# Performance work log

Measured on AMD Instinct MI355X. Metric: run time of the kernel, lower is better.

The kernel has to match this reference:

```python
import jax, jax.numpy as jnp
import numpy as np

T = 2048      # number of utterances in the dialogue (sequential loop dim)
L = 50        # tokens per utterance
V = 30000     # vocab size
D = 300       # word embedding dim
NF = 64       # CNN filters per width
H = 100       # hidden size (hard-coded in CMN)
NC = 7        # emotion classes
WIND = 40     # args.wind1 sliding memory window
HOPS = 3      # args.hops
NEG = -1e10   # masked_fill value in dotprod_attention


def setup_inputs() -> dict:
    key = jax.random.key(0)
    ks = jax.random.split(key, 24)
    s = 0.05

    def n(k, shape):
        return jax.random.normal(k, shape, jnp.float32) * s

    return {
        "sents": jax.random.randint(ks[0], (T, L), 0, V, dtype=jnp.int32),
        "lengths": jax.random.randint(ks[1], (T,), 1, L, dtype=jnp.int32),
        "emb": n(ks[2], (V, D)),
        "Wc3": n(ks[3], (NF, 1, 3, D)), "bc3": n(ks[4], (NF,)),
        "Wc4": n(ks[5], (NF, 1, 4, D)), "bc4": n(ks[6], (NF,)),
        "Wc5": n(ks[7], (NF, 1, 5, D)), "bc5": n(ks[8], (NF,)),
        "Wt": n(ks[9], (3 * NF, H)), "bt": n(ks[10], (H,)),
        "Wih_c": n(ks[11], (3 * H, H)), "Whh_c": n(ks[12], (3 * H, H)),
        "bih_c": n(ks[13], (3 * H,)), "bhh_c": n(ks[14], (3 * H,)),
        "Wih_m": n(ks[15], (3 * H, H)), "Whh_m": n(ks[16], (3 * H, H)),
        "bih_m": n(ks[17], (3 * H,)), "bhh_m": n(ks[18], (3 * H,)),
        "Wcls": n(ks[19], (H, NC)), "bcls": n(ks[20], (NC,)),
    }


def _gru_cell(x, h, Wih, Whh, bih, bhh):
    # torch GRU cell, gate order (r, z, n)
    gi = x @ Wih.T + bih
    gh = h @ Whh.T + bhh
    ir, iz, inn = jnp.split(gi, 3, axis=-1)
    hr, hz, hn = jnp.split(gh, 3, axis=-1)
    r = jax.nn.sigmoid(ir + hr)
    z = jax.nn.sigmoid(iz + hz)
    nw = jnp.tanh(inn + r * hn)
    return (1.0 - z) * nw + z * h


def reference(sents, lengths, emb, Wc3, bc3, Wc4, bc4, Wc5, bc5, Wt, bt,
              Wih_c, Whh_c, bih_c, bhh_c, Wih_m, Whh_m, bih_m, bhh_m,
              Wcls, bcls):
    # ---- CNN utterance encoder (dropout layers are identity in eval) ----
    w = emb[sents]                       # (T, L, D)
    x = w[:, None]                       # (T, 1, L, D)  NCHW
    feats = []
    for Wc, bc in ((Wc3, bc3), (Wc4, bc4), (Wc5, bc5)):
        y = jax.lax.conv_general_dilated(
            x, Wc, window_strides=(1, 1), padding='VALID',
            dimension_numbers=('NCHW', 'OIHW', 'NCHW'))  # (T, NF, L-fs+1, 1)
        feats.append(jnp.max(jax.nn.relu(y + bc[None, :, None, None]), axis=(2, 3)))
    s_utt = jnp.tanh(jnp.concatenate(feats, axis=1) @ Wt + bt)  # (T, H)

    # ---- context GRU over utterances 0..T-2 (hidden after torch step i is hiddens[i-1]) ----
    def cont_step(h, u):
        h2 = _gru_cell(u, h, Wih_c, Whh_c, bih_c, bhh_c)
        return h2, h2
    _, hiddens = jax.lax.scan(cont_step, jnp.zeros((H,), jnp.float32), s_utt[:-1])  # (T-1, H)

    # ---- sliding memory windows: step i (1..T-1) sees hiddens[i-WIND .. i-1], newest last ----
    idx = jnp.arange(1, T)[:, None] - WIND + jnp.arange(WIND)[None, :]  # (T-1, WIND)
    valid = idx >= 0
    mem_all = jnp.where(valid[..., None], hiddens[jnp.clip(idx, 0)], 0.0)  # (T-1, WIND, H)

    def attend(query, mem, v):
        # query: (H,), mem: (WIND, H), v: (WIND,) bool
        for _ in range(HOPS):
            scores = jnp.where(v, mem @ query, NEG)
            a = jax.nn.softmax(scores)
            query = jnp.tanh(query + a @ mem)
            if HOPS > 1:
                # mem_gru over the valid suffix of the window (zero init hidden,
                # padded slots skipped so recurrence starts at first valid slot)
                def mstep(hm, xv):
                    xx, vv = xv
                    hn = _gru_cell(xx, hm, Wih_m, Whh_m, bih_m, bhh_m)
                    hm = jnp.where(vv, hn, hm)
                    return hm, hm
                _, mem = jax.lax.scan(mstep, jnp.zeros((H,), jnp.float32), (mem, v))
        return query

    queries = jax.vmap(attend)(s_utt[1:], mem_all, valid)       # (T-1, H)
    s_cont = jnp.concatenate([s_utt[:1], queries], axis=0)      # (T, H)
    logits = s_cont @ Wcls + bcls                                # (T, NC)
    return jax.nn.log_softmax(logits, axis=1)
```

## Files before the change

kernel.cpp:

```cpp
#include <hip/hip_runtime.h>

#define TT 2048
#define LL 50
#define DD 300
#define HH 100
#define NCC 7

typedef unsigned short u16;
typedef unsigned int u32;
typedef _Float16 f16x2 __attribute__((ext_vector_type(2)));
typedef _Float16 f16x8 __attribute__((ext_vector_type(8)));
typedef float f32x4 __attribute__((ext_vector_type(4)));

__device__ __forceinline__ float frcp(float x){ return __builtin_amdgcn_rcpf(x); }
__device__ __forceinline__ float sigm(float x){ return frcp(1.f + __expf(-x)); }
__device__ __forceinline__ float ftanh(float x){ return 1.f - 2.f * frcp(1.f + __expf(2.f * x)); }

#if defined(__has_builtin)
#if __has_builtin(__builtin_amdgcn_fdot2)
#define HAS_FDOT2 1
#endif
#endif
__device__ __forceinline__ float fdot2(f16x2 a, f16x2 b, float c){
#ifdef HAS_FDOT2
  return __builtin_amdgcn_fdot2(a, b, c, false);
#else
  return c + (float)a.x * (float)b.x + (float)a.y * (float)b.y;
#endif
}
__device__ __forceinline__ f16x2 pk(float x, float y){ f16x2 r; r.x = (_Float16)x; r.y = (_Float16)y; return r; }

__global__ __launch_bounds__(256) void k_prep(const float* __restrict__ Wc3,
    const float* __restrict__ Wc4, const float* __restrict__ Wc5, _Float16* __restrict__ wtp)
{
  const int t = blockIdx.x;
  int kki, ntile, kt;
  if (t < 120){ kki = 0; ntile = t / 30;        kt = t % 30; }
  else if (t < 280){ kki = 1; int r = t - 120; ntile = r / 40; kt = r % 40; }
  else { kki = 2; int r = t - 280;             ntile = r / 50; kt = r % 50; }
  const float* W = (kki == 0) ? Wc3 : ((kki == 1) ? Wc4 : Wc5);
  const int kk = 3 + kki;
  #pragma unroll
  for (int u = 0; u < 2; ++u){
    int e = threadIdx.x * 2 + u;
    int lane = e >> 3, i = e & 7;
    int k = kt * 32 + (lane >> 4) * 8 + i;
    int f = ntile * 16 + (lane & 15);
    int j = k / 320, d = k - j * 320;
    float v = (d < DD) ? W[((size_t)f * kk + j) * DD + d] : 0.f;
    wtp[(size_t)t * 512 + e] = (_Float16)v;
  }
}

#define WST 328
__global__ __launch_bounds__(256) void k_cnn(const int* __restrict__ sents,
    const float* __restrict__ emb, const _Float16* __restrict__ wtp,
    const float* __restrict__ bc3, const float* __restrict__ bc4, const float* __restrict__ bc5,
    const float* __restrict__ Wt,  const float* __restrict__ bt,
    float* __restrict__ su)
{
  __shared__ __attribute__((aligned(16))) _Float16 w16[52 * WST];
  __shared__ float feats[192];
  __shared__ int ids[LL];
  const int tid = threadIdx.x;
  const int s = blockIdx.x;

  if (tid < LL) ids[tid] = sents[s * LL + tid];
  for (int e = tid; e < 52 * WST / 2; e += 256) ((u32*)w16)[e] = 0u;
  __syncthreads();
  for (int e = tid; e < LL * 75; e += 256){
    int l = e / 75, d4 = (e - l * 75) * 4;
    float4 v = *(const float4*)&emb[(size_t)ids[l] * DD + d4];
    _Float16* p = &w16[l * WST + d4];
    p[0] = (_Float16)v.x; p[1] = (_Float16)v.y; p[2] = (_Float16)v.z; p[3] = (_Float16)v.w;
  }
  __syncthreads();

  const int lane = tid & 63, wid = tid >> 6;
  const int rl = lane & 15, gp = lane >> 4;
  const int kkstart[3] = {0, 120, 280};
  float fmaxv[3];
  #pragma unroll
  for (int kki = 0; kki < 3; ++kki){
    const int kk = 3 + kki, nkt = kk * 10, Pk = LL - kk + 1;
    f32x4 acc0 = {0.f,0.f,0.f,0.f}, acc1 = acc0, acc2 = acc0;
    const f16x8* bp = (const f16x8*)(wtp + (size_t)(kkstart[kki] + wid * nkt) * 512) + lane;
    int j = 0, d = gp * 8;
    for (int kt = 0; kt < nkt; ++kt){
      f16x8 b  = bp[(size_t)kt * 64];
      f16x8 a0 = *(const f16x8*)&w16[(rl      + j) * WST + d];
      f16x8 a1 = *(const f16x8*)&w16[(16 + rl + j) * WST + d];
      f16x8 a2 = *(const f16x8*)&w16[(32 + rl + j) * WST + d];
      acc0 = __builtin_amdgcn_mfma_f32_16x16x32_f16(a0, b, acc0, 0, 0, 0);
      acc1 = __builtin_amdgcn_mfma_f32_16x16x32_f16(a1, b, acc1, 0, 0, 0);
      acc2 = __builtin_amdgcn_mfma_f32_16x16x32_f16(a2, b, acc2, 0, 0, 0);
      d += 32; if (d >= 320){ d -= 320; ++j; }
    }
    float m = -1e30f;
    #pragma unroll
    for (int r = 0; r < 4; ++r){
      int p0 = gp * 4 + r;
      if (p0 < Pk)      m = fmaxf(m, acc0[r]);
      if (16 + p0 < Pk) m = fmaxf(m, acc1[r]);
      if (32 + p0 < Pk) m = fmaxf(m, acc2[r]);
    }
    m = fmaxf(m, __shfl_xor(m, 16));
    m = fmaxf(m, __shfl_xor(m, 32));
    fmaxv[kki] = m;
  }
  if (lane < 16){
    feats[  0 + wid * 16 + lane] = fmaxv[0];
    feats[ 64 + wid * 16 + lane] = fmaxv[1];
    feats[128 + wid * 16 + lane] = fmaxv[2];
  }
  __syncthreads();
  if (tid < 192){
    float bias = (tid < 64) ? bc3[tid] : ((tid < 128) ? bc4[tid - 64] : bc5[tid - 128]);
    feats[tid] = fmaxf(0.f, feats[tid] + bias);
  }
  __syncthreads();
  if (tid < HH){
    float acc = bt[tid];
    for (int c = 0; c < 192; ++c)
      acc += feats[c] * Wt[c * HH + tid];
    su[(size_t)s * HH + tid] = ftanh(acc);
  }
}

__global__ __launch_bounds__(320) void k_gi(const float* __restrict__ src,
    const float* __restrict__ W, const float* __restrict__ b, float* __restrict__ dst)
{
  __shared__ float x[HH];
  const int t = blockIdx.x, tid = threadIdx.x;
  if (tid < HH) x[tid] = src[(size_t)t * HH + tid];
  __syncthreads();
  if (tid < 300){
    float acc = b[tid];
    const float* wr = W + (size_t)tid * HH;
    #pragma unroll
    for (int i = 0; i < 25; ++i){
      float4 wv = *(const float4*)(wr + 4 * i);
      float4 xv = *(const float4*)&x[4 * i];
      acc += xv.x * wv.x + xv.y * wv.y + xv.z * wv.z + xv.w * wv.w;
    }
    dst[(size_t)t * 300 + tid] = acc;
  }
}

#define CH 16
__global__ __launch_bounds__(320, 1) void k_scan(const float* __restrict__ gi,
    const float* __restrict__ Whh, const float* __restrict__ bhh,
    float* __restrict__ hid, int steps)
{
  __shared__ __attribute__((aligned(16))) _Float16 h16[104];
  __shared__ float gh_l[300];
  __shared__ float gi_buf[CH * 300];
  __shared__ float hid_buf[CH * HH];
  const int tid = threadIdx.x;
  f16x2 wv[52];
  float bh = 0.f, hreg = 0.f;
  if (tid < 300){
    const float* r0 = Whh + (size_t)tid * 100;
    #pragma unroll
    for (int i = 0; i < 25; ++i){
      float4 a = *(const float4*)(r0 + 4 * i);
      wv[2*i] = pk(a.x, a.y); wv[2*i+1] = pk(a.z, a.w);
    }
    bh = bhh[tid];
  }
  wv[50] = pk(0,0); wv[51] = pk(0,0);
  if (tid < 104) h16[tid] = (_Float16)0.f;
  {
    int c0 = (steps < CH ? steps : CH) * 75;
    for (int e = tid; e < c0; e += 320)
      ((float4*)gi_buf)[e] = ((const float4*)gi)[e];
  }
  __syncthreads();

  int t0 = 0;
  while (t0 < steps){
    int cnt = steps - t0; if (cnt > CH) cnt = CH;
    for (int s = 0; s < cnt; ++s){
      if (tid < 300){
        float a0 = 0, a1 = 0;
        const float4* hq = (const float4*)h16;
        #pragma unroll
        for (int g = 0; g < 13; ++g){
          float4 hv = hq[g];
          a0 = fdot2(wv[4*g  ], __builtin_bit_cast(f16x2, hv.x), a0);
          a1 = fdot2(wv[4*g+1], __builtin_bit_cast(f16x2, hv.y), a1);
          a0 = fdot2(wv[4*g+2], __builtin_bit_cast(f16x2, hv.z), a0);
          a1 = fdot2(wv[4*g+3], __builtin_bit_cast(f16x2, hv.w), a1);
        }
        gh_l[tid] = a0 + a1 + bh;
      }
      __syncthreads();
      if (tid < HH){
        const float* gp = gi_buf + s * 300;
        float r = sigm(gp[tid]       + gh_l[tid]);
        float z = sigm(gp[tid + 100] + gh_l[tid + 100]);
        float n = ftanh(gp[tid + 200] + r * gh_l[tid + 200]);
        float o = (1.f - z) * n + z * hreg;
        hreg = o;
        h16[tid] = (_Float16)o;
        hid_buf[s * HH + tid] = o;
      }
      __syncthreads();
    }
    for (int e = tid; e < cnt * 25; e += 320)
      ((float4*)(hid + (size_t)t0 * HH))[e] = ((const float4*)hid_buf)[e];
    int nt0 = t0 + cnt;
    int ncnt = steps - nt0; if (ncnt > CH) ncnt = CH; if (ncnt < 0) ncnt = 0;
    for (int e = tid; e < ncnt * 75; e += 320)
      ((float4*)gi_buf)[e] = ((const float4*)(gi + (size_t)nt0 * 300))[e];
    __syncthreads();
    t0 = nt0;
  }
}

__global__ __launch_bounds__(320) void k_att(
    const float* __restrict__ su, const float* __restrict__ hid, const float* __restrict__ gm,
    const float* __restrict__ Wih, const float* __restrict__ Whh,
    const float* __restrict__ bih, const float* __restrict__ bhh,
    float* __restrict__ scont)
{
  __shared__ float mem_l[40 * 104];
  __shared__ __attribute__((aligned(16))) _Float16 mem16[40 * 104];
  __shared__ float hbuf[HH];
  __shared__ __attribute__((aligned(16))) _Float16 hb16[104];
  __shared__ float gh_l[300];
  __shared__ float q_l[104];
  __shared__ float sc_l[40];
  __shared__ float bi_l[300];
  __shared__ _Float16 g_l[40 * 300];
  const int tid = threadIdx.x;
  const int q = blockIdx.x;
  int wmin = 39 - q; if (wmin < 0) wmin = 0;
  f16x2 wreg[52];
  float bh = 0.f;

  if (tid < 300){ bi_l[tid] = bih[tid]; bh = bhh[tid]; }
  if (tid < 104) q_l[tid] = (tid < 100) ? su[(size_t)(q + 1) * HH + tid] : 0.f;
  for (int e = tid; e < 40 * 104; e += 320){
    int w = e / 104, i = e - w * 104;
    float v = 0.f;
    if (i < 100 && w >= wmin) v = hid[(size_t)(q - 39 + w) * HH + i];
    mem_l[e] = v;
    mem16[e] = (_Float16)v;
  }
  for (int e = tid; e < 40 * 300; e += 320){
    int w = e / 300, j = e - w * 300;
    float v = (w >= wmin) ? gm[(size_t)(q - 39 + w) * 300 + j] : 0.f;
    g_l[e] = (_Float16)v;
  }
  if (tid < 300){
    const float* r0 = Whh + (size_t)tid * 100;
    #pragma unroll
    for (int i = 0; i < 25; ++i){
      float4 a = *(const float4*)(r0 + 4 * i);
      wreg[2*i] = pk(a.x, a.y); wreg[2*i+1] = pk(a.z, a.w);
    }
  }
  wreg[50] = pk(0,0); wreg[51] = pk(0,0);
  __syncthreads();

  for (int hop = 0; hop < 3; ++hop){
    if (tid < 40){
      float a0 = 0, a1 = 0, a2 = 0, a3 = 0;
      const float* mr = &mem_l[tid * 104];
      #pragma unroll
      for (int i = 0; i < 25; ++i){
        float4 m4 = *(const float4*)&mr[4 * i];
        float4 q4 = *(const float4*)&q_l[4 * i];
        a0 += m4.x * q4.x; a1 += m4.y * q4.y; a2 += m4.z * q4.z; a3 += m4.w * q4.w;
      }
      sc_l[tid] = (tid >= wmin) ? ((a0 + a1) + (a2 + a3)) : -1e10f;
    }
    __syncthreads();
    if (tid < 64){
      float v = (tid < 40) ? sc_l[tid] : -3e38f;
      float m = v;
      #pragma unroll
      for (int off = 32; off; off >>= 1) m = fmaxf(m, __shfl_xor(m, off));
      float e = (tid < 40) ? __expf(v - m) : 0.f;
      float ssum = e;
      #pragma unroll
      for (int off = 32; off; off >>= 1) ssum += __shfl_xor(ssum, off);
      if (tid < 40) sc_l[tid] = e * frcp(ssum);
    }
    __syncthreads();
    if (tid < 50){
      float c0 = 0.f, c1 = 0.f;
      for (int w = wmin; w < 40; ++w){
        float a = sc_l[w];
        float2 mv = *(const float2*)&mem_l[w * 104 + 2 * tid];
        c0 += a * mv.x; c1 += a * mv.y;
      }
      float q0 = ftanh(q_l[2 * tid]     + c0);
      float q1 = ftanh(q_l[2 * tid + 1] + c1);
      *(float2*)&q_l[2 * tid] = make_float2(q0, q1);
      if (hop == 2)
        *(float2*)&scont[(size_t)(q + 1) * HH + 2 * tid] = make_float2(q0, q1);
    }
    if (hop == 2) break;

    if (hop == 1){
      if (tid < 300){
        const float* r0 = Wih + (size_t)tid * 100;
        #pragma unroll
        for (int i = 0; i < 25; ++i){
          float4 a = *(const float4*)(r0 + 4 * i);
          wreg[2*i] = pk(a.x, a.y); wreg[2*i+1] = pk(a.z, a.w);
        }
        for (int w = 0; w < 40; ++w){
          float a0 = 0, a1 = 0;
          const float4* mq = (const float4*)&mem16[w * 104];
          #pragma unroll
          for (int g = 0; g < 13; ++g){
            float4 hv = mq[g];
            a0 = fdot2(wreg[4*g  ], __builtin_bit_cast(f16x2, hv.x), a0);
            a1 = fdot2(wreg[4*g+1], __builtin_bit_cast(f16x2, hv.y), a1);
            a0 = fdot2(wreg[4*g+2], __builtin_bit_cast(f16x2, hv.z), a0);
            a1 = fdot2(wreg[4*g+3], __builtin_bit_cast(f16x2, hv.w), a1);
          }
          g_l[w * 300 + tid] = (_Float16)(a0 + a1 + bi_l[tid]);
        }
        const float* rh = Whh + (size_t)tid * 100;
        #pragma unroll
        for (int i = 0; i < 25; ++i){
          float4 a = *(const float4*)(rh + 4 * i);
          wreg[2*i] = pk(a.x, a.y); wreg[2*i+1] = pk(a.z, a.w);
        }
      }
    }

    if (tid < HH) hbuf[tid] = 0.f;
    if (tid < 104) hb16[tid] = (_Float16)0.f;
    __syncthreads();
    for (int w = 0; w < 40; ++w){
      if (tid < 300){
        float a0 = 0, a1 = 0;
        const float4* hq = (const float4*)hb16;
        #pragma unroll
        for (int g = 0; g < 13; ++g){
          float4 hv = hq[g];
          a0 = fdot2(wreg[4*g  ], __builtin_bit_cast(f16x2, hv.x), a0);
          a1 = fdot2(wreg[4*g+1], __builtin_bit_cast(f16x2, hv.y), a1);
          a0 = fdot2(wreg[4*g+2], __builtin_bit_cast(f16x2, hv.z), a0);
          a1 = fdot2(wreg[4*g+3], __builtin_bit_cast(f16x2, hv.w), a1);
        }
        gh_l[tid] = a0 + a1 + bh;
      }
      __syncthreads();
      if (tid < HH){
        float o = hbuf[tid];
        if (w >= wmin){
          const _Float16* gp = &g_l[w * 300];
          float gir = (float)gp[tid], giz = (float)gp[tid + 100], gin = (float)gp[tid + 200];
          float r = sigm(gir + gh_l[tid]);
          float z = sigm(giz + gh_l[tid + 100]);
          float n = ftanh(gin + r * gh_l[tid + 200]);
          o = (1.f - z) * n + z * o;
        }
        hbuf[tid] = o;
        hb16[tid] = (_Float16)o;
        mem_l[w * 104 + tid] = o;
        mem16[w * 104 + tid] = (_Float16)o;
      }
      __syncthreads();
    }
  }
}

__global__ __launch_bounds__(256) void k_cls(const float* __restrict__ su, const float* __restrict__ scont,
    const float* __restrict__ Wcls, const float* __restrict__ bcls, float* __restrict__ out)
{
  __shared__ float wl[HH * NCC];
  __shared__ float bl[NCC];
  const int tid = threadIdx.x;
  for (int e = tid; e < HH * NCC; e += 256) wl[e] = Wcls[e];
  if (tid < NCC) bl[tid] = bcls[tid];
  __syncthreads();
  int r = blockIdx.x * 256 + tid;
  if (r < TT){
    const float* v = (r == 0) ? su : (scont + (size_t)r * HH);
    float l[NCC];
    #pragma unroll
    for (int c = 0; c < NCC; ++c) l[c] = bl[c];
    for (int h = 0; h < HH; ++h){
      float x = v[h];
      #pragma unroll
      for (int c = 0; c < NCC; ++c) l[c] += x * wl[h * NCC + c];
    }
    float m = l[0];
    #pragma unroll
    for (int c = 1; c < NCC; ++c) m = fmaxf(m, l[c]);
    float ssum = 0.f;
    #pragma unroll
    for (int c = 0; c < NCC; ++c) ssum += __expf(l[c] - m);
    float lse = m + __logf(ssum);
    #pragma unroll
    for (int c = 0; c < NCC; ++c) out[(size_t)r * NCC + c] = l[c] - lse;
  }
}

extern "C" void kernel_launch(void* const* d_in, const int* in_sizes, int n_in,
                              void* d_out, int out_size, void* d_ws, size_t ws_size,
                              hipStream_t stream)
{
  const int* sents  = (const int*)d_in[0];
  const float* emb    = (const float*)d_in[2];
  const float* Wc3    = (const float*)d_in[3];  const float* bc3 = (const float*)d_in[4];
  const float* Wc4    = (const float*)d_in[5];  const float* bc4 = (const float*)d_in[6];
  const float* Wc5    = (const float*)d_in[7];  const float* bc5 = (const float*)d_in[8];
  const float* Wt     = (const float*)d_in[9];  const float* bt  = (const float*)d_in[10];
  const float* Wih_c  = (const float*)d_in[11]; const float* Whh_c = (const float*)d_in[12];
  const float* bih_c  = (const float*)d_in[13]; const float* bhh_c = (const float*)d_in[14];
  const float* Wih_m  = (const float*)d_in[15]; const float* Whh_m = (const float*)d_in[16];
  const float* bih_m  = (const float*)d_in[17]; const float* bhh_m = (const float*)d_in[18];
  const float* Wcls   = (const float*)d_in[19]; const float* bcls  = (const float*)d_in[20];

  float* ws    = (float*)d_ws;
  float* su    = ws;
  float* gic   = su  + 204800;
  float* hid   = gic + 614100;
  float* gm    = gic;
  float* scont = hid + 204700;
  _Float16* wtp = (_Float16*)(scont + 204800);

  k_prep<<<480,     256, 0, stream>>>(Wc3, Wc4, Wc5, wtp);
  k_cnn <<<TT,      256, 0, stream>>>(sents, emb, wtp, bc3, bc4, bc5, Wt, bt, su);
  k_gi  <<<TT - 1,  320, 0, stream>>>(su, Wih_c, bih_c, gic);
  k_scan<<<1,       320, 0, stream>>>(gic, Whh_c, bhh_c, hid, TT - 1);
  k_gi  <<<TT - 1,  320, 0, stream>>>(hid, Wih_m, bih_m, gm);
  k_att <<<TT - 1,  320, 0, stream>>>(su, hid, gm, Wih_m, Whh_m, bih_m, bhh_m, scont);
  k_cls <<<(TT + 255) / 256, 256, 0, stream>>>(su, scont, Wcls, bcls, (float*)d_out);
}
```

Measured before the change: 1.996 ms.

## Remap GRU scan lanes so gates exchange via DPP, one barrier per step

The sequential GRU scan kernel now places the r/z/n gate rows for one hidden unit in adjacent lanes of a quad, using 448 threads. Gate values are exchanged with DPP quad broadcasts instead of going through shared memory. The hidden-state buffer is double-buffered, so each timestep needs one __syncthreads instead of two. This targets barrier and LDS round-trip latency on the serial critical path, at the cost of more threads and redundant gate math in idle lanes.

```diff
diff --git a/kernel.cpp b/kernel.cpp
--- a/kernel.cpp
+++ b/kernel.cpp
@@ -29,6 +29,12 @@
 #endif
 }
 __device__ __forceinline__ f16x2 pk(float x, float y){ f16x2 r; r.x = (_Float16)x; r.y = (_Float16)y; return r; }
+
+template<int CTRL>
+__device__ __forceinline__ float qb(float x){
+  return __builtin_bit_cast(float,
+    __builtin_amdgcn_mov_dpp(__builtin_bit_cast(int, x), CTRL, 0xF, 0xF, true));
+}
 
 __global__ __launch_bounds__(256) void k_prep(const float* __restrict__ Wc3,
     const float* __restrict__ Wc4, const float* __restrict__ Wc5, _Float16* __restrict__ wtp)
@@ -148,31 +154,36 @@
 }
 
 #define CH 16
-__global__ __launch_bounds__(320, 1) void k_scan(const float* __restrict__ gi,
+__global__ __launch_bounds__(448, 1) void k_scan(const float* __restrict__ gi,
     const float* __restrict__ Whh, const float* __restrict__ bhh,
     float* __restrict__ hid, int steps)
 {
-  __shared__ __attribute__((aligned(16))) _Float16 h16[104];
-  __shared__ float gh_l[300];
+  __shared__ __attribute__((aligned(16))) _Float16 hA[104];
+  __shared__ __attribute__((aligned(16))) _Float16 hB[104];
   __shared__ float gi_buf[CH * 300];
   __shared__ float hid_buf[CH * HH];
   const int tid = threadIdx.x;
+  const int w = tid >> 6, l = tid & 63;
+  const int u = w * 16 + (l >> 2), g = l & 3;
+  const bool act = (u < HH) && (g < 3);
+  const int row = act ? (u + 100 * g) : 0;
+  const int gidx = act ? (u + 100 * g) : 0;
   f16x2 wv[52];
   float bh = 0.f, hreg = 0.f;
-  if (tid < 300){
-    const float* r0 = Whh + (size_t)tid * 100;
+  {
+    const float* r0 = Whh + (size_t)row * 100;
     #pragma unroll
     for (int i = 0; i < 25; ++i){
       float4 a = *(const float4*)(r0 + 4 * i);
       wv[2*i] = pk(a.x, a.y); wv[2*i+1] = pk(a.z, a.w);
     }
-    bh = bhh[tid];
+    bh = bhh[row];
   }
   wv[50] = pk(0,0); wv[51] = pk(0,0);
-  if (tid < 104) h16[tid] = (_Float16)0.f;
+  if (tid < 104){ hA[tid] = (_Float16)0.f; hB[tid] = (_Float16)0.f; }
   {
     int c0 = (steps < CH ? steps : CH) * 75;
-    for (int e = tid; e < c0; e += 320)
+    for (int e = tid; e < c0; e += 448)
       ((float4*)gi_buf)[e] = ((const float4*)gi)[e];
   }
   __syncthreads();
@@ -181,37 +192,38 @@
   while (t0 < steps){
     int cnt = steps - t0; if (cnt > CH) cnt = CH;
     for (int s = 0; s < cnt; ++s){
-      if (tid < 300){
-        float a0 = 0, a1 = 0;
-        const float4* hq = (const float4*)h16;
-        #pragma unroll
-        for (int g = 0; g < 13; ++g){
-          float4 hv = hq[g];
-          a0 = fdot2(wv[4*g  ], __builtin_bit_cast(f16x2, hv.x), a0);
-          a1 = fdot2(wv[4*g+1], __builtin_bit_cast(f16x2, hv.y), a1);
-          a0 = fdot2(wv[4*g+2], __builtin_bit_cast(f16x2, hv.z), a0);
-          a1 = fdot2(wv[4*g+3], __builtin_bit_cast(f16x2, hv.w), a1);
-        }
-        gh_l[tid] = a0 + a1 + bh;
+      const _Float16* hs = ((t0 + s) & 1) ? hB : hA;
+      _Float16*       hd = ((t0 + s) & 1) ? hA : hB;
+      float giv = gi_buf[s * 300 + gidx];
+      float a0 = 0, a1 = 0;
+      const float4* hq = (const float4*)hs;
+      #pragma unroll
+      for (int gg = 0; gg < 13; ++gg){
+        float4 hv = hq[gg];
+        a0 = fdot2(wv[4*gg  ], __builtin_bit_cast(f16x2, hv.x), a0);
+        a1 = fdot2(wv[4*gg+1], __builtin_bit_cast(f16x2, hv.y), a1);
+        a0 = fdot2(wv[4*gg+2], __builtin_bit_cast(f16x2, hv.z), a0);
+        a1 = fdot2(wv[4*gg+3], __builtin_bit_cast(f16x2, hv.w), a1);
+      }
+      float gh = a0 + a1 + bh;
+      float ghr = qb<0x00>(gh),  ghz = qb<0x55>(gh),  ghn = qb<0xAA>(gh);
+      float gir = qb<0x00>(giv), giz = qb<0x55>(giv), gin = qb<0xAA>(giv);
+      float r = sigm(gir + ghr);
+      float z = sigm(giz + ghz);
+      float n = ftanh(gin + r * ghn);
+      float o = (1.f - z) * n + z * hreg;
+      hreg = o;
+      if (g == 0 && u < HH){
+        hd[u] = (_Float16)o;
+        hid_buf[s * HH + u] = o;
       }
       __syncthreads();
-      if (tid < HH){
-        const float* gp = gi_buf + s * 300;
-        float r = sigm(gp[tid]       + gh_l[tid]);
-        float z = sigm(gp[tid + 100] + gh_l[tid + 100]);
-        float n = ftanh(gp[tid + 200] + r * gh_l[tid + 200]);
-        float o = (1.f - z) * n + z * hreg;
-        hreg = o;
-        h16[tid] = (_Float16)o;
-        hid_buf[s * HH + tid] = o;
-      }
-      __syncthreads();
-    }
-    for (int e = tid; e < cnt * 25; e += 320)
+    }
+    for (int e = tid; e < cnt * 25; e += 448)
       ((float4*)(hid + (size_t)t0 * HH))[e] = ((const float4*)hid_buf)[e];
     int nt0 = t0 + cnt;
     int ncnt = steps - nt0; if (ncnt > CH) ncnt = CH; if (ncnt < 0) ncnt = 0;
-    for (int e = tid; e < ncnt * 75; e += 320)
+    for (int e = tid; e < ncnt * 75; e += 448)
       ((float4*)gi_buf)[e] = ((const float4*)(gi + (size_t)nt0 * 300))[e];
     __syncthreads();
     t0 = nt0;
@@ -431,7 +443,7 @@
   k_prep<<<480,     256, 0, stream>>>(Wc3, Wc4, Wc5, wtp);
   k_cnn <<<TT,      256, 0, stream>>>(sents, emb, wtp, bc3, bc4, bc5, Wt, bt, su);
   k_gi  <<<TT - 1,  320, 0, stream>>>(su, Wih_c, bih_c, gic);
-  k_scan<<<1,       320, 0, stream>>>(gic, Whh_c, bhh_c, hid, TT - 1);
+  k_scan<<<1,       448, 0, stream>>>(gic, Whh_c, bhh_c, hid, TT - 1);
   k_gi  <<<TT - 1,  320, 0, stream>>>(hid, Wih_m, bih_m, gm);
   k_att <<<TT - 1,  320, 0, stream>>>(su, hid, gm, Wih_m, Whh_m, bih_m, bhh_m, scont);
   k_cls <<<(TT + 255) / 256, 256, 0, stream>>>(su, scont, Wcls, bcls, (float*)d_out);
```

Measured after the change: 2.997 ms. +50.2%, slower.

## Compute GRU hidden matvec in scan with MFMA and double chunk size

Applied to the files above, without the earlier changes.

The sequential GRU scan kernel now computes the Whh·h matvec with MFMA 16x16x32 f16 instructions. The weight matrix is held as A fragments spread over 5 waves × 4 M-tiles, and h is broadcast as the B operand, replacing the per-thread fdot2 loops. Bias is added later in the gate stage, and the gi staging chunk grows from 16 to 32 steps to reduce refill syncs. MFMA on a matrix-vector product wastes 15 of 16 columns, and its latency on the serial critical path may not beat the dot-product version.

```diff
diff --git a/kernel.cpp b/kernel.cpp
--- a/kernel.cpp
+++ b/kernel.cpp
@@ -147,29 +147,39 @@
   }
 }
 
-#define CH 16
+#define CH 32
 __global__ __launch_bounds__(320, 1) void k_scan(const float* __restrict__ gi,
     const float* __restrict__ Whh, const float* __restrict__ bhh,
     float* __restrict__ hid, int steps)
 {
-  __shared__ __attribute__((aligned(16))) _Float16 h16[104];
-  __shared__ float gh_l[300];
+  __shared__ __attribute__((aligned(16))) _Float16 h16[128];
+  __shared__ __attribute__((aligned(16))) float gh_l[304];
   __shared__ float gi_buf[CH * 300];
   __shared__ float hid_buf[CH * HH];
   const int tid = threadIdx.x;
-  f16x2 wv[52];
-  float bh = 0.f, hreg = 0.f;
-  if (tid < 300){
-    const float* r0 = Whh + (size_t)tid * 100;
-    #pragma unroll
-    for (int i = 0; i < 25; ++i){
-      float4 a = *(const float4*)(r0 + 4 * i);
-      wv[2*i] = pk(a.x, a.y); wv[2*i+1] = pk(a.z, a.w);
-    }
-    bh = bhh[tid];
-  }
-  wv[50] = pk(0,0); wv[51] = pk(0,0);
-  if (tid < 104) h16[tid] = (_Float16)0.f;
+  const int lane = tid & 63, wvid = tid >> 6;
+  const int rl = lane & 15, gp = lane >> 4;
+
+  f16x8 afrag[4][4];
+  #pragma unroll
+  for (int m = 0; m < 4; ++m){
+    int mt = wvid + 5 * m;
+    int row = mt * 16 + rl;
+    #pragma unroll
+    for (int kt = 0; kt < 4; ++kt){
+      f16x8 f;
+      #pragma unroll
+      for (int i = 0; i < 8; ++i){
+        int k = kt * 32 + gp * 8 + i;
+        float v = (row < 300 && k < 100) ? Whh[(size_t)row * 100 + k] : 0.f;
+        f[i] = (_Float16)v;
+      }
+      afrag[m][kt] = f;
+    }
+  }
+  float bhr = 0.f, bhz = 0.f, bhn = 0.f, hreg = 0.f;
+  if (tid < HH){ bhr = bhh[tid]; bhz = bhh[tid + 100]; bhn = bhh[tid + 200]; }
+  if (tid < 128) h16[tid] = (_Float16)0.f;
   {
     int c0 = (steps < CH ? steps : CH) * 75;
     for (int e = tid; e < c0; e += 320)
@@ -181,25 +191,27 @@
   while (t0 < steps){
     int cnt = steps - t0; if (cnt > CH) cnt = CH;
     for (int s = 0; s < cnt; ++s){
-      if (tid < 300){
-        float a0 = 0, a1 = 0;
-        const float4* hq = (const float4*)h16;
+      {
+        const f16x8* hp = (const f16x8*)h16;
+        f16x8 bf0 = hp[ 0 + gp], bf1 = hp[ 4 + gp], bf2 = hp[ 8 + gp], bf3 = hp[12 + gp];
         #pragma unroll
-        for (int g = 0; g < 13; ++g){
-          float4 hv = hq[g];
-          a0 = fdot2(wv[4*g  ], __builtin_bit_cast(f16x2, hv.x), a0);
-          a1 = fdot2(wv[4*g+1], __builtin_bit_cast(f16x2, hv.y), a1);
-          a0 = fdot2(wv[4*g+2], __builtin_bit_cast(f16x2, hv.z), a0);
-          a1 = fdot2(wv[4*g+3], __builtin_bit_cast(f16x2, hv.w), a1);
-        }
-        gh_l[tid] = a0 + a1 + bh;
+        for (int m = 0; m < 4; ++m){
+          f32x4 acc = {0.f, 0.f, 0.f, 0.f};
+          acc = __builtin_amdgcn_mfma_f32_16x16x32_f16(afrag[m][0], bf0, acc, 0, 0, 0);
+          acc = __builtin_amdgcn_mfma_f32_16x16x32_f16(afrag[m][1], bf1, acc, 0, 0, 0);
+          acc = __builtin_amdgcn_mfma_f32_16x16x32_f16(afrag[m][2], bf2, acc, 0, 0, 0);
+          acc = __builtin_amdgcn_mfma_f32_16x16x32_f16(afrag[m][3], bf3, acc, 0, 0, 0);
+          int mt = wvid + 5 * m;
+          if (rl == 0 && mt < 19)
+            *(float4*)&gh_l[mt * 16 + gp * 4] = *(float4*)&acc;
+        }
       }
       __syncthreads();
       if (tid < HH){
-        const float* gp = gi_buf + s * 300;
-        float r = sigm(gp[tid]       + gh_l[tid]);
-        float z = sigm(gp[tid + 100] + gh_l[tid + 100]);
-        float n = ftanh(gp[tid + 200] + r * gh_l[tid + 200]);
+        const float* gpp = gi_buf + s * 300;
+        float r = sigm(gpp[tid]       + gh_l[tid]       + bhr);
+        float z = sigm(gpp[tid + 100] + gh_l[tid + 100] + bhz);
+        float n = ftanh(gpp[tid + 200] + r * (gh_l[tid + 200] + bhn));
         float o = (1.f - z) * n + z * hreg;
         hreg = o;
         h16[tid] = (_Float16)o;
```

New measurement: 2.011 ms. About the same (+0.8%).
